# Optimization experiments

Hardware: AMD Instinct MI355X
Metric: run time of the kernel (lower is better)

The kernel has to match this reference:

```python
import jax, jax.numpy as jnp
import numpy as np

BASIS_PRIMES = (2, 3, 5, 7, 11, 13, 17, 19, 23, 29)


def _build_resonance(max_seq):
    # p-adic valuations v_p(n) for n = 1..max_seq, each basis prime (vectorized LUT build)
    n = np.arange(1, max_seq + 1, dtype=np.int64)
    vals = np.zeros((max_seq, len(BASIS_PRIMES)), dtype=np.float32)
    for j, p in enumerate(BASIS_PRIMES):
        m = n.copy()
        while True:
            div = (m % p) == 0
            if not div.any():
                break
            vals[div, j] += 1.0
            m = np.where(div, m // p, m)
    # resonance(a,b) = sum_i min(v_{p_i}(a), v_{p_i}(b))  -> [T, T]
    res = np.zeros((max_seq, max_seq), dtype=np.float32)
    for j in range(len(BASIS_PRIMES)):
        vj = vals[:, j]
        res += np.minimum(vj[:, None], vj[None, :])
    causal = np.tril(np.ones((max_seq, max_seq), dtype=bool))
    allowed = ((res > 0) | np.eye(max_seq, dtype=bool)) & causal
    bias = (np.log1p(res) * allowed).astype(np.float32)
    return bias, allowed


def setup_inputs() -> dict:
    B, T, d_model, head_size, max_seq = 8, 2048, 1024, 128, 2048
    key = jax.random.key(0)
    kx, kq, kk, kv = jax.random.split(key, 4)
    bound = 1.0 / np.sqrt(d_model)  # torch Linear default init range
    x = jax.random.normal(kx, (B, T, d_model), dtype=jnp.float32)
    Wq = jax.random.uniform(kq, (head_size, d_model), jnp.float32, -bound, bound)
    Wk = jax.random.uniform(kk, (head_size, d_model), jnp.float32, -bound, bound)
    Wv = jax.random.uniform(kv, (head_size, d_model), jnp.float32, -bound, bound)
    bias, allowed = _build_resonance(max_seq)
    return {
        "x": x, "Wq": Wq, "Wk": Wk, "Wv": Wv,
        "resonance_bias": jnp.asarray(bias),
        "allowed": jnp.asarray(allowed),
    }


def reference(x, Wq, Wk, Wv, resonance_bias, allowed):
    B, T, C = x.shape
    q = jnp.einsum('btc,hc->bth', x, Wq)
    k = jnp.einsum('btc,hc->bth', x, Wk)
    v = jnp.einsum('btc,hc->bth', x, Wv)
    # NOTE: original scales by C**-0.5 where C = d_model (input channels)
    wei = jnp.einsum('bth,bsh->bts', q, k) * (C ** -0.5)
    wei = wei + resonance_bias[:T, :T]
    neg = jnp.finfo(wei.dtype).min
    wei = jnp.where(allowed[:T, :T], wei, neg)
    wei = jax.nn.softmax(wei, axis=-1)  # dropout is identity in eval mode
    return jnp.einsum('bts,bsh->bth', wei, v)
```

## Files before the change

### kernel.cpp

```cpp
#include <hip/hip_runtime.h>
#include <hip/hip_bf16.h>
#include <stdint.h>

typedef float f32x4  __attribute__((ext_vector_type(4)));
typedef short s16x8  __attribute__((ext_vector_type(8)));
typedef short s16x4  __attribute__((ext_vector_type(4)));
typedef unsigned short u16x8 __attribute__((ext_vector_type(8)));

#define MFMA16(A,B,C) __builtin_amdgcn_mfma_f32_16x16x32_bf16((A),(B),(C),0,0,0)

__device__ __forceinline__ short f2bf(float f) {
    uint32_t u = __float_as_uint(f);
    u += 0x7FFFu + ((u >> 16) & 1u);
    return (short)(u >> 16);
}
__device__ __forceinline__ float bf2f(unsigned short u) {
    return __uint_as_float(((uint32_t)u) << 16);
}
__device__ __forceinline__ int cum_jobs(int qt) {
  int h = qt >> 1;
  return (qt & 1) ? (h + 1) * (h + 1) : h * (h + 1);
}

#define OFF_PB   0u
#define OFF_WPK  8388608u
#define OFF_PQ   9175040u
#define OFF_PK   13369344u
#define OFF_PV   17563648u
#define OFF_XPK  21757952u
#define OFF_PML  21757952u
#define OFF_PO   22863872u
#define WS_SPLIT 60096512u

__global__ __launch_bounds__(256) void pack_all_kernel(
    const float* __restrict__ wq, const float* __restrict__ wk,
    const float* __restrict__ wv, const float* __restrict__ bias,
    const float* __restrict__ x, short* __restrict__ Wpk,
    short* __restrict__ pb, short* __restrict__ xpk) {
  const int tid = threadIdx.x, wid = tid >> 6, lane = tid & 63;
  const int g = lane >> 4, c4 = lane & 15;
  if (blockIdx.x < 192) {
    const int idx = blockIdx.x * 4 + wid;
    const int im = idx >> 8, rest = idx & 255;
    const int ntl = rest >> 5, k32 = rest & 31;
    const float* w = (im == 0) ? wq : (im == 1) ? wk : wv;
    const float* p = w + (size_t)(ntl * 16 + c4) * 1024 + k32 * 32 + 4 * g;
    f32x4 lo = *(const f32x4*)p;
    f32x4 hi = *(const f32x4*)(p + 16);
    s16x8 o = { f2bf(lo[0]), f2bf(lo[1]), f2bf(lo[2]), f2bf(lo[3]),
                f2bf(hi[0]), f2bf(hi[1]), f2bf(hi[2]), f2bf(hi[3]) };
    *(s16x8*)(Wpk + (size_t)idx * 512 + lane * 8) = o;
  } else if (blockIdx.x < 2240) {
    const int idx = (blockIdx.x - 192) * 4 + wid;
    const int t16 = idx >> 6, s32 = idx & 63;
    const int t = t16 * 16 + c4;
    const int sb = s32 * 32 + 4 * g;
    const float* p = bias + (size_t)t * 2048 + sb;
    f32x4 lo = *(const f32x4*)p;
    f32x4 hi = *(const f32x4*)(p + 16);
    s16x8 o;
    #pragma unroll
    for (int i = 0; i < 4; ++i) {
      int s0 = sb + i, s1 = sb + 16 + i;
      bool ok0 = (s0 <= t) && (s0 == t || lo[i] > 0.f);
      bool ok1 = (s1 <= t) && (s1 == t || hi[i] > 0.f);
      o[i]     = f2bf(ok0 ? lo[i] : -1e30f);
      o[4 + i] = f2bf(ok1 ? hi[i] : -1e30f);
    }
    *(s16x8*)(pb + (size_t)idx * 512 + lane * 8) = o;
  } else {
    const int idx = (blockIdx.x - 2240) * 4 + wid;
    const int m16 = idx >> 5, k32 = idx & 31;
    const float* p = x + (size_t)(m16 * 16 + c4) * 1024 + k32 * 32 + 4 * g;
    f32x4 lo = *(const f32x4*)p;
    f32x4 hi = *(const f32x4*)(p + 16);
    s16x8 o = { f2bf(lo[0]), f2bf(lo[1]), f2bf(lo[2]), f2bf(lo[3]),
                f2bf(hi[0]), f2bf(hi[1]), f2bf(hi[2]), f2bf(hi[3]) };
    *(s16x8*)(xpk + (size_t)idx * 512 + lane * 8) = o;
  }
}

__global__ __launch_bounds__(256, 2) void qkv_gemm11_kernel(
    const short* __restrict__ xpk, const short* __restrict__ Wpk,
    short* __restrict__ pq, short* __restrict__ pk, short* __restrict__ pv) {
  __shared__ short lx[2][8192];
  const int tid = threadIdx.x, wid = tid >> 6, lane = tid & 63;
  const int g = lane >> 4, c4 = lane & 15;
  const int L8 = lane * 8;
  const int x8 = blockIdx.x & 7, q = blockIdx.x >> 3;
  const int im = q % 3, rt = (q / 3) * 8 + x8;
  const int b = rt >> 4;
  const int h = wid & 1, ch = wid >> 1;

#define G11_STAGE(buf, kk) { \
    _Pragma("unroll") \
    for (int i = 0; i < 4; ++i) { \
      const int fidx = wid * 4 + i; \
      const short* src = (fidx < 8) \
        ? xpk + (size_t)((rt * 8 + fidx) * 32 + (kk)) * 512 + L8 \
        : Wpk + (size_t)(im * 256 + (fidx - 8) * 32 + (kk)) * 512 + L8; \
      __builtin_amdgcn_global_load_lds( \
          (const __attribute__((address_space(1))) void*)src, \
          (__attribute__((address_space(3))) void*)&lx[buf][fidx * 512], \
          16, 0, 0); \
    } }

  f32x4 acc[4][4];
  #pragma unroll
  for (int tt = 0; tt < 4; ++tt)
    #pragma unroll
    for (int nn = 0; nn < 4; ++nn) acc[tt][nn] = (f32x4){0.f, 0.f, 0.f, 0.f};

  G11_STAGE(0, 0)
  __syncthreads();

  if (im < 2) {
    for (int k = 0; k < 32; ++k) {
      const int cur = k & 1;
      if (k < 31) G11_STAGE(cur ^ 1, k + 1)
      s16x8 af[4], bfr[4];
      #pragma unroll
      for (int tt = 0; tt < 4; ++tt)
        af[tt] = *(const s16x8*)&lx[cur][(h * 4 + tt) * 512 + L8];
      #pragma unroll
      for (int nn = 0; nn < 4; ++nn)
        bfr[nn] = *(const s16x8*)&lx[cur][(8 + ch * 4 + nn) * 512 + L8];
      #pragma unroll
      for (int tt = 0; tt < 4; ++tt)
        #pragma unroll
        for (int nn = 0; nn < 4; ++nn)
          acc[tt][nn] = MFMA16(bfr[nn], af[tt], acc[tt][nn]);
      __syncthreads();
    }
    short* __restrict__ o = (im == 1) ? pk : pq;
    #pragma unroll
    for (int tt = 0; tt < 4; ++tt) {
      const int q16 = (rt & 15) * 8 + h * 4 + tt;
      #pragma unroll
      for (int fl = 0; fl < 2; ++fl) {
        const int f = ch * 2 + fl;
        s16x8 fr = { f2bf(acc[tt][2*fl][0]),   f2bf(acc[tt][2*fl][1]),
                     f2bf(acc[tt][2*fl][2]),   f2bf(acc[tt][2*fl][3]),
                     f2bf(acc[tt][2*fl+1][0]), f2bf(acc[tt][2*fl+1][1]),
                     f2bf(acc[tt][2*fl+1][2]), f2bf(acc[tt][2*fl+1][3]) };
        *(s16x8*)(o + (size_t)(b * 512 + q16 * 4 + f) * 512 + L8) = fr;
      }
    }
  } else {
    for (int k = 0; k < 32; ++k) {
      const int cur = k & 1;
      if (k < 31) G11_STAGE(cur ^ 1, k + 1)
      s16x8 af[4], bfr[4];
      #pragma unroll
      for (int tt = 0; tt < 4; ++tt)
        af[tt] = *(const s16x8*)&lx[cur][(h * 4 + tt) * 512 + L8];
      #pragma unroll
      for (int nn = 0; nn < 4; ++nn)
        bfr[nn] = *(const s16x8*)&lx[cur][(8 + ch * 4 + nn) * 512 + L8];
      #pragma unroll
      for (int tt = 0; tt < 4; ++tt)
        #pragma unroll
        for (int nn = 0; nn < 4; ++nn)
          acc[tt][nn] = MFMA16(af[tt], bfr[nn], acc[tt][nn]);
      __syncthreads();
    }
    #pragma unroll
    for (int pr = 0; pr < 2; ++pr) {
      const int s32 = (rt & 15) * 4 + h * 2 + pr;
      #pragma unroll
      for (int nn = 0; nn < 4; ++nn) {
        const int nt = ch * 4 + nn;
        s16x8 fr = { f2bf(acc[2*pr][nn][0]),   f2bf(acc[2*pr][nn][1]),
                     f2bf(acc[2*pr][nn][2]),   f2bf(acc[2*pr][nn][3]),
                     f2bf(acc[2*pr+1][nn][0]), f2bf(acc[2*pr+1][nn][1]),
                     f2bf(acc[2*pr+1][nn][2]), f2bf(acc[2*pr+1][nn][3]) };
        *(s16x8*)(pv + (size_t)(b * 512 + s32 * 8 + nt) * 512 + L8) = fr;
      }
    }
  }
#undef G11_STAGE
}

template<bool SPLIT>
__global__ __launch_bounds__(128) void attn_kernel(
    const short* __restrict__ pq, const short* __restrict__ pk,
    const short* __restrict__ pv, const short* __restrict__ pb,
    float* __restrict__ out, float* __restrict__ part_ml,
    short* __restrict__ part_o) {
  int qt, c;
  if (SPLIT) {
    const int i = blockIdx.x;
    int h = (int)sqrtf((float)i);
    while (h * h > i) --h;
    while ((h + 1) * (h + 1) <= i) ++h;
    if (i < h * (h + 1)) { qt = 2 * h - 1; c = i - h * h; }
    else                 { qt = 2 * h;     c = i - h * (h + 1); }
  } else {
    qt = blockIdx.x; c = 0;
  }
  const int n = (qt >> 1) + 1;
  const int tid = threadIdx.x;
  const int wid = tid >> 6, lane = tid & 63;
  const int g = lane >> 4, c4 = lane & 15;
  const int b = blockIdx.y;
  const int q16a = qt * 4 + wid * 2;
  const int L8 = lane * 8;

  s16x8 qfa[4], qfb[4];
  #pragma unroll
  for (int f = 0; f < 4; ++f) {
    qfa[f] = *(const s16x8*)(pq + (size_t)(b * 512 + q16a * 4 + f) * 512 + L8);
    qfb[f] = *(const s16x8*)(pq + (size_t)(b * 512 + (q16a + 1) * 4 + f) * 512 + L8);
  }

  float m0 = -1e30f, l0 = 0.f, m1 = -1e30f, l1 = 0.f;
  f32x4 acc0[8], acc1[8];
  #pragma unroll
  for (int i = 0; i < 8; ++i) {
    acc0[i] = (f32x4){0.f, 0.f, 0.f, 0.f};
    acc1[i] = (f32x4){0.f, 0.f, 0.f, 0.f};
  }

  const int q_hi_w = qt * 64 + wid * 32 + 32;
  const int s_begin = SPLIT ? c * 128 : 0;
  const int s_stop  = min(SPLIT ? s_begin + 128 : (1 << 30), q_hi_w);

  for (int s0 = s_begin; s0 < s_stop; s0 += 32) {
    const int s16i = s0 >> 4, s32 = s0 >> 5;
    const short* kbase = pk + (size_t)(b * 512 + s16i * 4) * 512 + L8;
    const short* vbase = pv + (size_t)(b * 512 + s32 * 8) * 512 + L8;
    s16x8 kf0[4], kf1[4];
    #pragma unroll
    for (int f = 0; f < 4; ++f) {
      kf0[f] = *(const s16x8*)(kbase + (size_t)f * 512);
      kf1[f] = *(const s16x8*)(kbase + (size_t)(4 + f) * 512);
    }
    u16x8 bva = *(const u16x8*)(pb + (size_t)(q16a * 64 + s32) * 512 + L8);
    u16x8 bvb = *(const u16x8*)(pb + (size_t)((q16a + 1) * 64 + s32) * 512 + L8);
    f32x4 s0a = (f32x4){0.f,0.f,0.f,0.f}, s1a = (f32x4){0.f,0.f,0.f,0.f};
    f32x4 s0b = (f32x4){0.f,0.f,0.f,0.f}, s1b = (f32x4){0.f,0.f,0.f,0.f};
    __builtin_amdgcn_s_setprio(1);
    #pragma unroll
    for (int f = 0; f < 4; ++f) {
      s0a = MFMA16(kf0[f], qfa[f], s0a);
      s1a = MFMA16(kf1[f], qfa[f], s1a);
      s0b = MFMA16(kf0[f], qfb[f], s0b);
      s1b = MFMA16(kf1[f], qfb[f], s1b);
    }
    __builtin_amdgcn_s_setprio(0);
    float va[8], vb[8];
    #pragma unroll
    for (int st = 0; st < 2; ++st)
      #pragma unroll
      for (int r = 0; r < 4; ++r) {
        va[st * 4 + r] = (st ? s1a[r] : s0a[r]) * 0.03125f + bf2f(bva[st * 4 + r]);
        vb[st * 4 + r] = (st ? s1b[r] : s0b[r]) * 0.03125f + bf2f(bvb[st * 4 + r]);
      }
    float mva = va[0], mvb = vb[0];
    #pragma unroll
    for (int i = 1; i < 8; ++i) { mva = fmaxf(mva, va[i]); mvb = fmaxf(mvb, vb[i]); }
    mva = fmaxf(mva, __shfl_xor(mva, 16)); mva = fmaxf(mva, __shfl_xor(mva, 32));
    mvb = fmaxf(mvb, __shfl_xor(mvb, 16)); mvb = fmaxf(mvb, __shfl_xor(mvb, 32));
    if (!__all((mva <= m0 + 8.f) && (mvb <= m1 + 8.f))) {
      float mn0 = fmaxf(m0, mva), mn1 = fmaxf(m1, mvb);
      float a0 = __expf(m0 - mn0), a1 = __expf(m1 - mn1);
      l0 *= a0; l1 *= a1; m0 = mn0; m1 = mn1;
      float ar0[4], ar1[4];
      #pragma unroll
      for (int r = 0; r < 4; ++r) {
        ar0[r] = __shfl(a0, (lane & 48) | (4 * g + r));
        ar1[r] = __shfl(a1, (lane & 48) | (4 * g + r));
      }
      #pragma unroll
      for (int nt = 0; nt < 8; ++nt)
        #pragma unroll
        for (int r = 0; r < 4; ++r) {
          acc0[nt][r] *= ar0[r];
          acc1[nt][r] *= ar1[r];
        }
    }
    float pa8[8], pb8[8], psa = 0.f, psb = 0.f;
    #pragma unroll
    for (int i = 0; i < 8; ++i) {
      pa8[i] = (va[i] > -1e29f) ? __expf(va[i] - m0) : 0.f;  psa += pa8[i];
      pb8[i] = (vb[i] > -1e29f) ? __expf(vb[i] - m1) : 0.f;  psb += pb8[i];
    }
    psa += __shfl_xor(psa, 16); psa += __shfl_xor(psa, 32); l0 += psa;
    psb += __shfl_xor(psb, 16); psb += __shfl_xor(psb, 32); l1 += psb;
    s16x8 paf = { f2bf(pa8[0]), f2bf(pa8[1]), f2bf(pa8[2]), f2bf(pa8[3]),
                  f2bf(pa8[4]), f2bf(pa8[5]), f2bf(pa8[6]), f2bf(pa8[7]) };
    s16x8 pbf = { f2bf(pb8[0]), f2bf(pb8[1]), f2bf(pb8[2]), f2bf(pb8[3]),
                  f2bf(pb8[4]), f2bf(pb8[5]), f2bf(pb8[6]), f2bf(pb8[7]) };
    __builtin_amdgcn_s_setprio(1);
    #pragma unroll
    for (int nt = 0; nt < 8; ++nt) {
      s16x8 vf = *(const s16x8*)(vbase + (size_t)nt * 512);
      acc0[nt] = MFMA16(paf, vf, acc0[nt]);
      acc1[nt] = MFMA16(pbf, vf, acc1[nt]);
    }
    __builtin_amdgcn_s_setprio(0);
  }

  if (!SPLIT || n == 1) {
    float li0 = 1.f / l0, li1 = 1.f / l1;
    float lr0[4], lr1[4];
    #pragma unroll
    for (int r = 0; r < 4; ++r) {
      lr0[r] = __shfl(li0, (lane & 48) | (4 * g + r));
      lr1[r] = __shfl(li1, (lane & 48) | (4 * g + r));
    }
    const int row0 = qt * 64 + wid * 32;
    #pragma unroll
    for (int nt = 0; nt < 8; ++nt)
      #pragma unroll
      for (int r = 0; r < 4; ++r) {
        out[(size_t)(b * 2048 + row0 + 4 * g + r) * 128 + 16 * nt + c4] =
            acc0[nt][r] * lr0[r];
        out[(size_t)(b * 2048 + row0 + 16 + 4 * g + r) * 128 + 16 * nt + c4] =
            acc1[nt][r] * lr1[r];
      }
  } else {
    const int slot = b * 270 + cum_jobs(qt) - 2 + c;
    short* po = part_o + (size_t)slot * 8192 + (size_t)(wid * 8) * 512 + L8;
    #pragma unroll
    for (int nt = 0; nt < 8; ++nt) {
      s16x8 fr = { f2bf(acc0[nt][0]), f2bf(acc0[nt][1]),
                   f2bf(acc0[nt][2]), f2bf(acc0[nt][3]),
                   f2bf(acc1[nt][0]), f2bf(acc1[nt][1]),
                   f2bf(acc1[nt][2]), f2bf(acc1[nt][3]) };
      *(s16x8*)(po + (size_t)nt * 512) = fr;
    }
    if (lane < 16) {
      part_ml[slot * 128 + wid * 32 + c4]           = m0;
      part_ml[slot * 128 + wid * 32 + 16 + c4]      = m1;
      part_ml[slot * 128 + 64 + wid * 32 + c4]      = l0;
      part_ml[slot * 128 + 64 + wid * 32 + 16 + c4] = l1;
    }
  }
}

__global__ __launch_bounds__(256) void combine_kernel(
    const float* __restrict__ part_ml, const unsigned short* __restrict__ part_o,
    float* __restrict__ out) {
  const int qt = 2 + blockIdx.x;
  const int b = blockIdx.y;
  const int n = (qt >> 1) + 1;
  const int slot0 = b * 270 + cum_jobs(qt) - 2;
  const int tid = threadIdx.x;

  __shared__ float scl[16][64];
  if (tid < 64) {
    const int r = tid;
    float M = -1e30f;
    for (int cc = 0; cc < n; ++cc)
      M = fmaxf(M, part_ml[(size_t)(slot0 + cc) * 128 + r]);
    float L = 0.f;
    for (int cc = 0; cc < n; ++cc)
      L += part_ml[(size_t)(slot0 + cc) * 128 + 64 + r] *
           __expf(part_ml[(size_t)(slot0 + cc) * 128 + r] - M);
    float inv = 1.f / L;
    for (int cc = 0; cc < n; ++cc)
      scl[cc][r] = __expf(part_ml[(size_t)(slot0 + cc) * 128 + r] - M) * inv;
  }
  __syncthreads();
  const int fgr = tid >> 6, lane = tid & 63;
  const int g = lane >> 4, c4 = lane & 15;
  for (int ff = fgr; ff < 16; ff += 4) {
    const int rbase = (ff >> 3) * 32 + 4 * g;
    const int col = (ff & 7) * 16 + c4;
    float o[8] = {0.f,0.f,0.f,0.f,0.f,0.f,0.f,0.f};
    for (int cc = 0; cc < n; ++cc) {
      u16x8 v = *(const u16x8*)(part_o +
          (size_t)(slot0 + cc) * 8192 + (size_t)ff * 512 + lane * 8);
      #pragma unroll
      for (int j = 0; j < 8; ++j)
        o[j] += bf2f(v[j]) * scl[cc][rbase + (j >> 2) * 16 + (j & 3)];
    }
    #pragma unroll
    for (int j = 0; j < 8; ++j) {
      const int row = rbase + (j >> 2) * 16 + (j & 3);
      out[(size_t)(b * 2048 + qt * 64 + row) * 128 + col] = o[j];
    }
  }
}

extern "C" void kernel_launch(void* const* d_in, const int* in_sizes, int n_in,
                              void* d_out, int out_size, void* d_ws, size_t ws_size,
                              hipStream_t stream) {
  const float* x    = (const float*)d_in[0];
  const float* wq   = (const float*)d_in[1];
  const float* wk   = (const float*)d_in[2];
  const float* wv   = (const float*)d_in[3];
  const float* bias = (const float*)d_in[4];

  char* ws = (char*)d_ws;
  short* pb      = (short*)(ws + OFF_PB);
  short* Wpk     = (short*)(ws + OFF_WPK);
  short* pq      = (short*)(ws + OFF_PQ);
  short* pk      = (short*)(ws + OFF_PK);
  short* pv      = (short*)(ws + OFF_PV);
  short* xpk     = (short*)(ws + OFF_XPK);
  float* part_ml = (float*)(ws + OFF_PML);
  short* part_o  = (short*)(ws + OFF_PO);
  float* outp    = (float*)d_out;

  pack_all_kernel<<<10432, 256, 0, stream>>>(wq, wk, wv, bias, x, Wpk, pb, xpk);
  qkv_gemm11_kernel<<<384, 256, 0, stream>>>(xpk, Wpk, pq, pk, pv);

  if (ws_size >= WS_SPLIT) {
    attn_kernel<true><<<dim3(272, 8), 128, 0, stream>>>(
        pq, pk, pv, pb, outp, part_ml, part_o);
    combine_kernel<<<dim3(30, 8), 256, 0, stream>>>(
        part_ml, (const unsigned short*)part_o, outp);
  } else {
    attn_kernel<false><<<dim3(32, 8), 128, 0, stream>>>(
        pq, pk, pv, pb, outp, part_ml, part_o);
  }
}
```

Before: 94.83 us.

## Fuse x fp32-to-bf16 conversion into QKV GEMM, drop separate x packing pass

Removes the x-packing stage from the pack kernel and has the QKV GEMM stream fp32 x tiles straight into LDS, converting them to bf16 in registers with v_cvt_pk_bf16_f32 before the MFMAs. This saves the write and re-read of a 32MB bf16 copy of x, leaving only the fp32 read. In exchange LDS per block grows to 48KB, each x tile is converted once per block that reuses it (three projections), and the global-to-LDS traffic for x is doubled versus bf16. The rounding mode of the hardware conversion may differ slightly from the manual round-to-nearest-even.

Result: slower. 97.19 us (+2.5%).

```diff
diff --git a/kernel.cpp b/kernel.cpp
--- a/kernel.cpp
+++ b/kernel.cpp
@@ -16,6 +16,11 @@
 }
 __device__ __forceinline__ float bf2f(unsigned short u) {
     return __uint_as_float(((uint32_t)u) << 16);
+}
+__device__ __forceinline__ uint32_t cvtpk(float a, float b) {
+  uint32_t r;
+  asm("v_cvt_pk_bf16_f32 %0, %1, %2" : "=v"(r) : "v"(a), "v"(b));
+  return r;
 }
 __device__ __forceinline__ int cum_jobs(int qt) {
   int h = qt >> 1;
@@ -27,16 +32,14 @@
 #define OFF_PQ   9175040u
 #define OFF_PK   13369344u
 #define OFF_PV   17563648u
-#define OFF_XPK  21757952u
 #define OFF_PML  21757952u
 #define OFF_PO   22863872u
 #define WS_SPLIT 60096512u
 
-__global__ __launch_bounds__(256) void pack_all_kernel(
+__global__ __launch_bounds__(256) void pack_misc_kernel(
     const float* __restrict__ wq, const float* __restrict__ wk,
     const float* __restrict__ wv, const float* __restrict__ bias,
-    const float* __restrict__ x, short* __restrict__ Wpk,
-    short* __restrict__ pb, short* __restrict__ xpk) {
+    short* __restrict__ Wpk, short* __restrict__ pb) {
   const int tid = threadIdx.x, wid = tid >> 6, lane = tid & 63;
   const int g = lane >> 4, c4 = lane & 15;
   if (blockIdx.x < 192) {
@@ -50,7 +53,7 @@
     s16x8 o = { f2bf(lo[0]), f2bf(lo[1]), f2bf(lo[2]), f2bf(lo[3]),
                 f2bf(hi[0]), f2bf(hi[1]), f2bf(hi[2]), f2bf(hi[3]) };
     *(s16x8*)(Wpk + (size_t)idx * 512 + lane * 8) = o;
-  } else if (blockIdx.x < 2240) {
+  } else {
     const int idx = (blockIdx.x - 192) * 4 + wid;
     const int t16 = idx >> 6, s32 = idx & 63;
     const int t = t16 * 16 + c4;
@@ -68,22 +71,13 @@
       o[4 + i] = f2bf(ok1 ? hi[i] : -1e30f);
     }
     *(s16x8*)(pb + (size_t)idx * 512 + lane * 8) = o;
-  } else {
-    const int idx = (blockIdx.x - 2240) * 4 + wid;
-    const int m16 = idx >> 5, k32 = idx & 31;
-    const float* p = x + (size_t)(m16 * 16 + c4) * 1024 + k32 * 32 + 4 * g;
-    f32x4 lo = *(const f32x4*)p;
-    f32x4 hi = *(const f32x4*)(p + 16);
-    s16x8 o = { f2bf(lo[0]), f2bf(lo[1]), f2bf(lo[2]), f2bf(lo[3]),
-                f2bf(hi[0]), f2bf(hi[1]), f2bf(hi[2]), f2bf(hi[3]) };
-    *(s16x8*)(xpk + (size_t)idx * 512 + lane * 8) = o;
-  }
-}
-
-__global__ __launch_bounds__(256, 2) void qkv_gemm11_kernel(
-    const short* __restrict__ xpk, const short* __restrict__ Wpk,
+  }
+}
+
+__global__ __launch_bounds__(256, 2) void qkv_gemm12_kernel(
+    const float* __restrict__ x, const short* __restrict__ Wpk,
     short* __restrict__ pq, short* __restrict__ pk, short* __restrict__ pv) {
-  __shared__ short lx[2][8192];
+  __shared__ short lx[2][12288];
   const int tid = threadIdx.x, wid = tid >> 6, lane = tid & 63;
   const int g = lane >> 4, c4 = lane & 15;
   const int L8 = lane * 8;
@@ -92,17 +86,26 @@
   const int b = rt >> 4;
   const int h = wid & 1, ch = wid >> 1;
 
-#define G11_STAGE(buf, kk) { \
+#define G12_STAGE(buf, kk) { \
     _Pragma("unroll") \
-    for (int i = 0; i < 4; ++i) { \
-      const int fidx = wid * 4 + i; \
-      const short* src = (fidx < 8) \
-        ? xpk + (size_t)((rt * 8 + fidx) * 32 + (kk)) * 512 + L8 \
-        : Wpk + (size_t)(im * 256 + (fidx - 8) * 32 + (kk)) * 512 + L8; \
-      __builtin_amdgcn_global_load_lds( \
-          (const __attribute__((address_space(1))) void*)src, \
-          (__attribute__((address_space(3))) void*)&lx[buf][fidx * 512], \
-          16, 0, 0); \
+    for (int i = 0; i < 6; ++i) { \
+      const int u = wid * 6 + i; \
+      if (u < 16) { \
+        const int a = u >> 1, hf = u & 1; \
+        const float* src = x + (size_t)(rt * 128 + a * 16 + c4) * 1024 \
+                         + (size_t)(kk) * 32 + 4 * g + hf * 16; \
+        __builtin_amdgcn_global_load_lds( \
+            (const __attribute__((address_space(1))) void*)src, \
+            (__attribute__((address_space(3))) void*)&lx[buf][(2*a+hf)*512], \
+            16, 0, 0); \
+      } else { \
+        const int n = u - 16; \
+        const short* src = Wpk + (size_t)(im * 256 + n * 32 + (kk)) * 512 + L8; \
+        __builtin_amdgcn_global_load_lds( \
+            (const __attribute__((address_space(1))) void*)src, \
+            (__attribute__((address_space(3))) void*)&lx[buf][8192 + n * 512], \
+            16, 0, 0); \
+      } \
     } }
 
   f32x4 acc[4][4];
@@ -111,27 +114,40 @@
     #pragma unroll
     for (int nn = 0; nn < 4; ++nn) acc[tt][nn] = (f32x4){0.f, 0.f, 0.f, 0.f};
 
-  G11_STAGE(0, 0)
+  G12_STAGE(0, 0)
   __syncthreads();
 
+  union CV { uint32_t u[4]; s16x8 v; };
+
+#define G12_BODY(SWAPPED)                                                    \
+  for (int k = 0; k < 32; ++k) {                                             \
+    const int cur = k & 1;                                                   \
+    if (k < 31) G12_STAGE(cur ^ 1, k + 1)                                    \
+    s16x8 af[4], bfr[4];                                                     \
+    _Pragma("unroll")                                                        \
+    for (int tt = 0; tt < 4; ++tt) {                                         \
+      const int a = h * 4 + tt;                                              \
+      f32x4 alo = *(const f32x4*)&lx[cur][(2 * a) * 512 + L8];               \
+      f32x4 ahi = *(const f32x4*)&lx[cur][(2 * a + 1) * 512 + L8];           \
+      CV t;                                                                  \
+      t.u[0] = cvtpk(alo[0], alo[1]); t.u[1] = cvtpk(alo[2], alo[3]);        \
+      t.u[2] = cvtpk(ahi[0], ahi[1]); t.u[3] = cvtpk(ahi[2], ahi[3]);        \
+      af[tt] = t.v;                                                          \
+    }                                                                        \
+    _Pragma("unroll")                                                        \
+    for (int nn = 0; nn < 4; ++nn)                                           \
+      bfr[nn] = *(const s16x8*)&lx[cur][8192 + (ch * 4 + nn) * 512 + L8];    \
+    _Pragma("unroll")                                                        \
+    for (int tt = 0; tt < 4; ++tt)                                           \
+      _Pragma("unroll")                                                      \
+      for (int nn = 0; nn < 4; ++nn)                                         \
+        acc[tt][nn] = SWAPPED ? MFMA16(bfr[nn], af[tt], acc[tt][nn])         \
+                              : MFMA16(af[tt], bfr[nn], acc[tt][nn]);        \
+    __syncthreads();                                                         \
+  }
+
   if (im < 2) {
-    for (int k = 0; k < 32; ++k) {
-      const int cur = k & 1;
-      if (k < 31) G11_STAGE(cur ^ 1, k + 1)
-      s16x8 af[4], bfr[4];
-      #pragma unroll
-      for (int tt = 0; tt < 4; ++tt)
-        af[tt] = *(const s16x8*)&lx[cur][(h * 4 + tt) * 512 + L8];
-      #pragma unroll
-      for (int nn = 0; nn < 4; ++nn)
-        bfr[nn] = *(const s16x8*)&lx[cur][(8 + ch * 4 + nn) * 512 + L8];
-      #pragma unroll
-      for (int tt = 0; tt < 4; ++tt)
-        #pragma unroll
-        for (int nn = 0; nn < 4; ++nn)
-          acc[tt][nn] = MFMA16(bfr[nn], af[tt], acc[tt][nn]);
-      __syncthreads();
-    }
+    G12_BODY(1)
     short* __restrict__ o = (im == 1) ? pk : pq;
     #pragma unroll
     for (int tt = 0; tt < 4; ++tt) {
@@ -147,23 +163,7 @@
       }
     }
   } else {
-    for (int k = 0; k < 32; ++k) {
-      const int cur = k & 1;
-      if (k < 31) G11_STAGE(cur ^ 1, k + 1)
-      s16x8 af[4], bfr[4];
-      #pragma unroll
-      for (int tt = 0; tt < 4; ++tt)
-        af[tt] = *(const s16x8*)&lx[cur][(h * 4 + tt) * 512 + L8];
-      #pragma unroll
-      for (int nn = 0; nn < 4; ++nn)
-        bfr[nn] = *(const s16x8*)&lx[cur][(8 + ch * 4 + nn) * 512 + L8];
-      #pragma unroll
-      for (int tt = 0; tt < 4; ++tt)
-        #pragma unroll
-        for (int nn = 0; nn < 4; ++nn)
-          acc[tt][nn] = MFMA16(af[tt], bfr[nn], acc[tt][nn]);
-      __syncthreads();
-    }
+    G12_BODY(0)
     #pragma unroll
     for (int pr = 0; pr < 2; ++pr) {
       const int s32 = (rt & 15) * 4 + h * 2 + pr;
@@ -178,7 +178,8 @@
       }
     }
   }
-#undef G11_STAGE
+#undef G12_BODY
+#undef G12_STAGE
 }
 
 template<bool SPLIT>
@@ -399,13 +400,12 @@
   short* pq      = (short*)(ws + OFF_PQ);
   short* pk      = (short*)(ws + OFF_PK);
   short* pv      = (short*)(ws + OFF_PV);
-  short* xpk     = (short*)(ws + OFF_XPK);
   float* part_ml = (float*)(ws + OFF_PML);
   short* part_o  = (short*)(ws + OFF_PO);
   float* outp    = (float*)d_out;
 
-  pack_all_kernel<<<10432, 256, 0, stream>>>(wq, wk, wv, bias, x, Wpk, pb, xpk);
-  qkv_gemm11_kernel<<<384, 256, 0, stream>>>(xpk, Wpk, pq, pk, pv);
+  pack_misc_kernel<<<2240, 256, 0, stream>>>(wq, wk, wv, bias, Wpk, pb);
+  qkv_gemm12_kernel<<<384, 256, 0, stream>>>(x, Wpk, pq, pk, pv);
 
   if (ws_size >= WS_SPLIT) {
     attn_kernel<true><<<dim3(272, 8), 128, 0, stream>>>(
```
